# Kernel optimization log

Measured on AMD Instinct MI355X. Metric: run time of the kernel, lower is better.

## Reference

```python
import jax, jax.numpy as jnp
import numpy as np

L, T, B, N = 4, 8, 32, 65536          # layers, terms/layer, batch, flat weight size
D_K = D_V = 64; H = 8; RANK = 8       # from encoder_weight_spec
FEAT_IN = 7 * T * L                   # 224
OUT = D_K * RANK * H                  # 4096


def setup_inputs() -> dict:
    key = jax.random.key(0)
    ks = jax.random.split(key, 16)
    s = 0.05
    return {
        "wsfeat": jax.random.normal(ks[0], (L, T, B, 1, N), jnp.float32),
        "fn_W1": jax.random.normal(ks[1], (FEAT_IN, 64), jnp.float32) * s,
        "fn_b1": jnp.zeros((64,), jnp.float32),
        "ln_g": jnp.ones((64,), jnp.float32),
        "ln_b": jnp.zeros((64,), jnp.float32),
        "fn_W2": jax.random.normal(ks[2], (64, 32), jnp.float32) * s,
        "fn_b2": jnp.zeros((32,), jnp.float32),
        "MU_W": jax.random.normal(ks[3], (L, 32, OUT), jnp.float32) * s,
        "MU_b": jnp.zeros((L, OUT), jnp.float32),
        "MV_W": jax.random.normal(ks[4], (L, 32, OUT), jnp.float32) * s,
        "MV_b": jnp.zeros((L, OUT), jnp.float32),
        "NU_W": jax.random.normal(ks[5], (L, 32, OUT), jnp.float32) * s,
        "NU_b": jnp.zeros((L, OUT), jnp.float32),
        "NV_W": jax.random.normal(ks[6], (L, 32, OUT), jnp.float32) * s,
        "NV_b": jnp.zeros((L, OUT), jnp.float32),
    }


def _forward(wsfeat, fn_W1, fn_b1, ln_g, ln_b, fn_W2, fn_b2,
             MU_W, MU_b, MV_W, MV_b, NU_W, NU_b, NV_W, NV_b):
    quantiles = jnp.array([0.0, 0.25, 0.5, 0.75, 1.0], wsfeat.dtype)
    # per-term stats over last axis: mean, unbiased var, 5 linear-interp quantiles
    mean = wsfeat.mean(-1)                       # [L,T,B,1]
    var = wsfeat.var(-1, ddof=1)                 # torch.var default: unbiased
    q = jnp.quantile(wsfeat, quantiles, axis=-1)  # [5,L,T,B,1]
    feats = jnp.concatenate([mean[None], var[None], q], axis=0)  # [7,L,T,B,1]
    # original cat order: layer-major, then term, then the 7 stats
    x = jnp.transpose(feats, (3, 4, 1, 2, 0)).reshape(B, 1, L * T * 7)
    # feature_net: Linear -> LayerNorm -> GELU(exact) -> Linear
    h1 = x @ fn_W1 + fn_b1
    mu = h1.mean(-1, keepdims=True)
    v = h1.var(-1, keepdims=True)                # LayerNorm uses biased var
    h1 = (h1 - mu) / jnp.sqrt(v + 1e-5) * ln_g + ln_b
    h1 = jax.nn.gelu(h1, approximate=False)      # torch default GELU is exact erf
    feat = (h1 @ fn_W2 + fn_b2).reshape(B, 32)

    eye_scale = jnp.asarray(0.1, feat.dtype)

    def lowrank(UW, Ub, VW, Vb, D):
        # per-layer Linear(32 -> D*rank*h), vectorized over L
        U = (jnp.einsum('bf,lfo->lbo', feat, UW) + Ub[:, None, :]).reshape(L, B, H, D, RANK)
        V = (jnp.einsum('bf,lfo->lbo', feat, VW) + Vb[:, None, :]).reshape(L, B, H, RANK, D)
        M = jnp.einsum('lbhdr,lbhre->lbhde', U, V)
        return M + eye_scale * jnp.eye(D, dtype=feat.dtype)
    all_M = lowrank(MU_W, MU_b, MV_W, MV_b, D_K)  # [L,B,H,D_k,D_k]
    all_N = lowrank(NU_W, NU_b, NV_W, NV_b, D_V)  # [L,B,H,D_v,D_v]
    return all_M, all_N


def reference(wsfeat, fn_W1, fn_b1, ln_g, ln_b, fn_W2, fn_b2,
              MU_W, MU_b, MV_W, MV_b, NU_W, NU_b, NV_W, NV_b):
    return _forward(wsfeat, fn_W1, fn_b1, ln_g, ln_b, fn_W2, fn_b2,
                    MU_W, MU_b, MV_W, MV_b, NU_W, NU_b, NV_W, NV_b)
```

## Files before the change

kernel.cpp:

```cpp
#include <hip/hip_runtime.h>
#include <math.h>
#include <float.h>

#define SNT 512
#define NT 256
#define N_ROW 65536
#define B_ 32
#define L_ 4
#define T_ 8
#define H_ 8
#define OUT_ 4096
#define CAPW 2560
#define CAPB 512

#define LO0 -0.7095f
#define HI0 -0.6395f
#define LO1 -0.0350f
#define HI1  0.0350f
#define LO2  0.6395f
#define HI2  0.7095f
#define SBS (128.0f / 0.07f)

__device__ __forceinline__ unsigned f2k(float f) {
    unsigned u = __float_as_uint(f);
    return (u & 0x80000000u) ? ~u : (u | 0x80000000u);
}
__device__ __forceinline__ float k2f(unsigned k) {
    unsigned u = (k & 0x80000000u) ? (k ^ 0x80000000u) : ~k;
    return __uint_as_float(u);
}

__global__ __launch_bounds__(SNT, 8) void stats_kernel(const float* __restrict__ in,
                                                       float* __restrict__ x_ws) {
    const int row = blockIdx.x;
    const int tid = threadIdx.x;
    const int wid = tid >> 6;
    const int lane = tid & 63;
    const float4* __restrict__ p4 = (const float4*)(in + (size_t)row * N_ROW);

    __shared__ float cand[3][CAPW];
    __shared__ float bbuf[CAPB];
    __shared__ unsigned shist[128];
    __shared__ unsigned warpsum[8];
    __shared__ float4 redw[8];
    __shared__ int s_wcnt[3];
    __shared__ int s_cb[3];
    __shared__ int s_flag[6];
    __shared__ float s_qv[6];
    __shared__ int s_bc;
    __shared__ unsigned s_bidx, s_brem, s_bcnt;
    __shared__ unsigned s_dig, s_rdig;

    const unsigned ranks[6] = {16383u, 16384u, 32767u, 32768u, 49151u, 49152u};

    if (tid < 3) { s_wcnt[tid] = 0; s_cb[tid] = 0; }
    __syncthreads();

    float s = 0.f, s2 = 0.f, mn = FLT_MAX, mx = -FLT_MAX;
    int cb0 = 0, cb1 = 0, cb2 = 0;

    auto proc = [&](float x) {
        s += x; s2 = fmaf(x, x, s2);
        mn = fminf(mn, x); mx = fmaxf(mx, x);
        bool b0 = x < LO0, b1 = x < LO1, b2 = x < LO2;
        bool h0 = x < HI0, h1 = x < HI1, h2 = x < HI2;
        cb0 += b0; cb1 += b1; cb2 += b2;
        bool w0 = h0 && !b0, w1 = h1 && !b1, w2 = h2 && !b2;
        if (w0 || w1 || w2) {
            int w = w1 ? 1 : (w2 ? 2 : 0);
            int t = atomicAdd(&s_wcnt[w], 1);
            if (t < CAPW) cand[w][t] = x;
        }
    };

    for (int it = 0; it < N_ROW / 4 / SNT / 4; it++) {
        int base = it * 4 * SNT + tid;
        float4 v0 = p4[base];
        float4 v1 = p4[base + SNT];
        float4 v2 = p4[base + 2 * SNT];
        float4 v3 = p4[base + 3 * SNT];
        proc(v0.x); proc(v0.y); proc(v0.z); proc(v0.w);
        proc(v1.x); proc(v1.y); proc(v1.z); proc(v1.w);
        proc(v2.x); proc(v2.y); proc(v2.z); proc(v2.w);
        proc(v3.x); proc(v3.y); proc(v3.z); proc(v3.w);
    }

#pragma unroll
    for (int off = 32; off > 0; off >>= 1) {
        s += __shfl_xor(s, off);
        s2 += __shfl_xor(s2, off);
        mn = fminf(mn, __shfl_xor(mn, off));
        mx = fmaxf(mx, __shfl_xor(mx, off));
        cb0 += __shfl_xor(cb0, off);
        cb1 += __shfl_xor(cb1, off);
        cb2 += __shfl_xor(cb2, off);
    }
    if (lane == 0) {
        redw[wid] = make_float4(s, s2, mn, mx);
        atomicAdd(&s_cb[0], cb0);
        atomicAdd(&s_cb[1], cb1);
        atomicAdd(&s_cb[2], cb2);
    }
    __syncthreads();
    if (tid == 0) {
        float4 a = redw[0];
#pragma unroll
        for (int w = 1; w < 8; w++) {
            float4 b = redw[w];
            a.x += b.x; a.y += b.y;
            a.z = fminf(a.z, b.z); a.w = fmaxf(a.w, b.w);
        }
        redw[0] = a;
        for (int i = 0; i < 6; i++) {
            int w = i >> 1;
            long rl = (long)ranks[i] - (long)s_cb[w];
            int ok = (rl >= 0) && (rl < (long)s_wcnt[w]) && (s_wcnt[w] <= CAPW);
            s_flag[i] = !ok;
        }
    }
    __syncthreads();

    const float wlo[3] = {LO0, LO1, LO2};
    for (int w = 0; w < 3; w++) {
        if (s_flag[2 * w] && s_flag[2 * w + 1]) continue;
        int c = s_wcnt[w];
        float lo = wlo[w];
        if (tid < 128) shist[tid] = 0u;
        __syncthreads();
        for (int j = tid; j < c; j += SNT) {
            int sb = (int)((cand[w][j] - lo) * SBS);
            sb = sb < 0 ? 0 : (sb > 127 ? 127 : sb);
            atomicAdd(&shist[sb], 1u);
        }
        __syncthreads();
        if (wid == 0) {
            unsigned a0 = shist[2 * lane], a1 = shist[2 * lane + 1];
            unsigned t = a0 + a1, sc = t;
#pragma unroll
            for (int d = 1; d < 64; d <<= 1) {
                unsigned n = __shfl_up(sc, d);
                if (lane >= d) sc += n;
            }
            unsigned ex = sc - t;
            shist[2 * lane] = ex + a0;
            shist[2 * lane + 1] = ex + a0 + a1;
        }
        __syncthreads();
        for (int ii = 0; ii < 2; ii++) {
            int i = 2 * w + ii;
            if (s_flag[i]) continue;
            unsigned rl = ranks[i] - (unsigned)s_cb[w];
            if (tid < 128) {
                unsigned cc = shist[tid];
                unsigned cbp = tid ? shist[tid - 1] : 0u;
                if (rl < cc && rl >= cbp) {
                    s_bidx = (unsigned)tid; s_brem = rl - cbp; s_bcnt = cc - cbp;
                }
            }
            if (tid == 0) s_bc = 0;
            __syncthreads();
            if (s_bcnt > CAPB) {
                if (tid == 0) s_flag[i] = 1;
                __syncthreads();
                continue;
            }
            unsigned bidx = s_bidx;
            for (int j = tid; j < c; j += SNT) {
                float x = cand[w][j];
                int sb = (int)((x - lo) * SBS);
                sb = sb < 0 ? 0 : (sb > 127 ? 127 : sb);
                if ((unsigned)sb == bidx) { int q = atomicAdd(&s_bc, 1); bbuf[q] = x; }
            }
            __syncthreads();
            int bc = s_bc;
            unsigned rem = s_brem;
            for (int j = tid; j < bc; j += SNT) {
                float x = bbuf[j];
                int less = 0, eq = 0;
                for (int k = 0; k < bc; k++) {
                    float y = bbuf[k];
                    less += (y < x); eq += (y == x);
                }
                if ((unsigned)less <= rem && rem < (unsigned)(less + eq)) s_qv[i] = x;
            }
            __syncthreads();
        }
    }

    {
        unsigned* h2 = (unsigned*)&cand[0][0];
        for (int i = 0; i < 6; i++) {
            if (!s_flag[i]) continue;
            unsigned rank = ranks[i];
            unsigned prefix = 0;
            for (int level = 0; level < 3; level++) {
                int nb = (level == 2) ? 1024 : 2048;
                for (int j = tid; j < nb; j += SNT) h2[j] = 0u;
                __syncthreads();
                for (int j = tid; j < N_ROW / 4; j += SNT) {
                    float4 v = p4[j];
                    float xs[4] = {v.x, v.y, v.z, v.w};
#pragma unroll
                    for (int k = 0; k < 4; k++) {
                        unsigned key = f2k(xs[k]);
                        if (level == 0) atomicAdd(&h2[key >> 21], 1u);
                        else if (level == 1) { if ((key >> 21) == prefix) atomicAdd(&h2[(key >> 10) & 2047u], 1u); }
                        else { if ((key >> 10) == prefix) atomicAdd(&h2[key & 1023u], 1u); }
                    }
                }
                __syncthreads();
                int per = nb / SNT;
                unsigned ls[4]; unsigned acc = 0;
                int base = tid * per;
                for (int k = 0; k < per; k++) { acc += h2[base + k]; ls[k] = acc; }
                unsigned sc = acc;
#pragma unroll
                for (int d = 1; d < 64; d <<= 1) {
                    unsigned n = __shfl_up(sc, d);
                    if (lane >= d) sc += n;
                }
                if (lane == 63) warpsum[wid] = sc;
                __syncthreads();
                unsigned woff = 0;
                for (int ww = 0; ww < wid; ww++) woff += warpsum[ww];
                unsigned ex = woff + sc - acc;
                for (int k = 0; k < per; k++) h2[base + k] = ls[k] + ex;
                __syncthreads();
                for (int k = 0; k < per; k++) {
                    int j = base + k;
                    unsigned cc = h2[j];
                    unsigned cbp = j ? h2[j - 1] : 0u;
                    if (rank < cc && rank >= cbp) { s_dig = (unsigned)j; s_rdig = rank - cbp; }
                }
                __syncthreads();
                unsigned dig = s_dig;
                rank = s_rdig;
                prefix = (level == 0) ? dig : ((prefix << 11) | dig);
                __syncthreads();
            }
            if (tid == 0) s_qv[i] = k2f(prefix);
            __syncthreads();
        }
    }

    if (tid == 0) {
        double ssum = (double)redw[0].x;
        double ssq = (double)redw[0].y;
        float mean = (float)(ssum / 65536.0);
        float var = (float)((ssq - ssum * ssum / 65536.0) / 65535.0);
        float q25 = s_qv[0] + 0.75f * (s_qv[1] - s_qv[0]);
        float q50 = s_qv[2] + 0.5f * (s_qv[3] - s_qv[2]);
        float q75 = s_qv[4] + 0.25f * (s_qv[5] - s_qv[4]);
        int lt = row / B_;
        int b = row % B_;
        float* o = x_ws + b * 224 + lt * 7;
        o[0] = mean; o[1] = var; o[2] = redw[0].z;
        o[3] = q25;  o[4] = q50; o[5] = q75; o[6] = redw[0].w;
    }
}

__global__ __launch_bounds__(64) void featnet_kernel(
    const float* __restrict__ x_ws,
    const float* __restrict__ W1, const float* __restrict__ b1,
    const float* __restrict__ lng, const float* __restrict__ lnb,
    const float* __restrict__ W2, const float* __restrict__ b2,
    float* __restrict__ feat_ws) {
    int b = blockIdx.x;
    int j = threadIdx.x;
    __shared__ float xs[224];
    __shared__ float h1s[64];
    const float* x = x_ws + b * 224;
    for (int k = j; k < 224; k += 64) xs[k] = x[k];
    __syncthreads();
    float acc = b1[j];
    for (int k = 0; k < 224; k++) acc += xs[k] * W1[k * 64 + j];
    float s = acc, s2 = acc * acc;
    for (int off = 32; off > 0; off >>= 1) {
        s += __shfl_xor(s, off);
        s2 += __shfl_xor(s2, off);
    }
    float mu = s * (1.f / 64.f);
    float var = s2 * (1.f / 64.f) - mu * mu;
    float hn = (acc - mu) * rsqrtf(var + 1e-5f) * lng[j] + lnb[j];
    float ge = 0.5f * hn * (1.f + erff(hn * 0.70710678118654752f));
    h1s[j] = ge;
    __syncthreads();
    if (j < 32) {
        float a2 = b2[j];
        for (int k = 0; k < 64; k++) a2 += h1s[k] * W2[k * 32 + j];
        feat_ws[b * 32 + j] = a2;
    }
}

__global__ __launch_bounds__(NT) void lowrank_kernel(
    const float* __restrict__ feat,
    const float* __restrict__ MU_W, const float* __restrict__ MU_b,
    const float* __restrict__ MV_W, const float* __restrict__ MV_b,
    const float* __restrict__ NU_W, const float* __restrict__ NU_b,
    const float* __restrict__ NV_W, const float* __restrict__ NV_b,
    float* __restrict__ out) {
    int id = blockIdx.x;
    int l = id >> 8;
    int b = (id >> 3) & 31;
    int h = id & 7;
    int tid = threadIdx.x;

    __shared__ float fs[32];
    __shared__ float UM[512], VM[512], UN[512], VN[512];
    if (tid < 32) fs[tid] = feat[b * 32 + tid];
    __syncthreads();

    size_t woff = (size_t)l * 32 * OUT_ + (size_t)h * 512;
    size_t boff = (size_t)l * OUT_ + (size_t)h * 512;

    const float* Ws[4] = {MU_W, MV_W, NU_W, NV_W};
    const float* Bs[4] = {MU_b, MV_b, NU_b, NV_b};
    float* Ds[4] = {UM, VM, UN, VN};
#pragma unroll
    for (int m = 0; m < 4; m++) {
        const float* W = Ws[m] + woff;
        const float* Bv = Bs[m] + boff;
        float* D = Ds[m];
        for (int idx = tid; idx < 512; idx += NT) {
            float acc = Bv[idx];
#pragma unroll
            for (int f = 0; f < 32; f++) acc += fs[f] * W[(size_t)f * OUT_ + idx];
            D[idx] = acc;
        }
    }
    __syncthreads();

    int d = tid >> 2;
    int eb = (tid & 3) * 16;
    size_t obase = (size_t)id * 4096 + (size_t)d * 64 + eb;
    float* outN = out + (size_t)L_ * B_ * H_ * 4096;

    for (int e = 0; e < 16; e++) {
        float acc = 0.f;
#pragma unroll
        for (int r = 0; r < 8; r++) acc += UM[d * 8 + r] * VM[r * 64 + eb + e];
        if (d == eb + e) acc += 0.1f;
        out[obase + e] = acc;
    }
    for (int e = 0; e < 16; e++) {
        float acc = 0.f;
#pragma unroll
        for (int r = 0; r < 8; r++) acc += UN[d * 8 + r] * VN[r * 64 + eb + e];
        if (d == eb + e) acc += 0.1f;
        outN[obase + e] = acc;
    }
}

extern "C" void kernel_launch(void* const* d_in, const int* in_sizes, int n_in,
                              void* d_out, int out_size, void* d_ws, size_t ws_size,
                              hipStream_t stream) {
    const float* wsfeat = (const float*)d_in[0];
    const float* fn_W1 = (const float*)d_in[1];
    const float* fn_b1 = (const float*)d_in[2];
    const float* ln_g = (const float*)d_in[3];
    const float* ln_b = (const float*)d_in[4];
    const float* fn_W2 = (const float*)d_in[5];
    const float* fn_b2 = (const float*)d_in[6];
    const float* MU_W = (const float*)d_in[7];
    const float* MU_b = (const float*)d_in[8];
    const float* MV_W = (const float*)d_in[9];
    const float* MV_b = (const float*)d_in[10];
    const float* NU_W = (const float*)d_in[11];
    const float* NU_b = (const float*)d_in[12];
    const float* NV_W = (const float*)d_in[13];
    const float* NV_b = (const float*)d_in[14];

    float* x_ws = (float*)d_ws;
    float* feat_ws = x_ws + 32 * 224;

    stats_kernel<<<L_ * T_ * B_, SNT, 0, stream>>>(wsfeat, x_ws);
    featnet_kernel<<<B_, 64, 0, stream>>>(x_ws, fn_W1, fn_b1, ln_g, ln_b, fn_W2, fn_b2, feat_ws);
    lowrank_kernel<<<L_ * B_ * H_, NT, 0, stream>>>(feat_ws, MU_W, MU_b, MV_W, MV_b,
                                                    NU_W, NU_b, NV_W, NV_b, (float*)d_out);
}
```

Before: 113.2 us.

## Split row stats across segment blocks and batch U/V projection across batch

The per-row stats pass is split into four segment blocks per row, each writing partial sums, counts and window candidates to global workspace, and a second select kernel then merges them and does the quantile selection. This raises parallelism for the bandwidth-bound streaming pass. The low-rank stage is split into a uv_kernel that computes U/V for all batches from a shared-memory tile of weights, so each weight is read once per layer/column tile instead of once per batch, plus an expand kernel for the outer products. The cost is extra launches, a memset, global atomics, and round-trips through workspace.

```diff
diff --git a/kernel.cpp b/kernel.cpp
--- a/kernel.cpp
+++ b/kernel.cpp
@@ -2,15 +2,17 @@
 #include <math.h>
 #include <float.h>
 
-#define SNT 512
-#define NT 256
+#define TNT 256
 #define N_ROW 65536
+#define NSEG 4
+#define SEGN (N_ROW / NSEG)
 #define B_ 32
 #define L_ 4
 #define T_ 8
 #define H_ 8
 #define OUT_ 4096
 #define CAPW 2560
+#define CAPS 768
 #define CAPB 512
 
 #define LO0 -0.7095f
@@ -21,6 +23,14 @@
 #define HI2  0.7095f
 #define SBS (128.0f / 0.07f)
 
+#define XWS_OFF  0
+#define FEAT_OFF 7168
+#define PART_OFF 8192
+#define WCNT_OFF 40960
+#define CAND_OFF 49152
+#define UV_OFF   (49152 + 1024*3*CAPW)
+#define UV_MSTRIDE ((size_t)L_ * B_ * OUT_)
+
 __device__ __forceinline__ unsigned f2k(float f) {
     unsigned u = __float_as_uint(f);
     return (u & 0x80000000u) ? ~u : (u | 0x80000000u);
@@ -30,30 +40,25 @@
     return __uint_as_float(u);
 }
 
-__global__ __launch_bounds__(SNT, 8) void stats_kernel(const float* __restrict__ in,
-                                                       float* __restrict__ x_ws) {
-    const int row = blockIdx.x;
+__global__ __launch_bounds__(TNT) void stream_kernel(const float* __restrict__ in,
+                                                     float* __restrict__ ws) {
+    const int bid = blockIdx.x;
+    const int row = bid >> 2;
+    const int seg = bid & 3;
     const int tid = threadIdx.x;
     const int wid = tid >> 6;
     const int lane = tid & 63;
-    const float4* __restrict__ p4 = (const float4*)(in + (size_t)row * N_ROW);
-
-    __shared__ float cand[3][CAPW];
-    __shared__ float bbuf[CAPB];
-    __shared__ unsigned shist[128];
-    __shared__ unsigned warpsum[8];
-    __shared__ float4 redw[8];
-    __shared__ int s_wcnt[3];
-    __shared__ int s_cb[3];
-    __shared__ int s_flag[6];
-    __shared__ float s_qv[6];
-    __shared__ int s_bc;
-    __shared__ unsigned s_bidx, s_brem, s_bcnt;
-    __shared__ unsigned s_dig, s_rdig;
-
-    const unsigned ranks[6] = {16383u, 16384u, 32767u, 32768u, 49151u, 49152u};
-
-    if (tid < 3) { s_wcnt[tid] = 0; s_cb[tid] = 0; }
+    const float4* __restrict__ p4 =
+        (const float4*)(in + (size_t)row * N_ROW + (size_t)seg * SEGN);
+
+    __shared__ float cw[3][CAPS];
+    __shared__ int s_cnt[3];
+    __shared__ float4 redw[4];
+    __shared__ int redc[4][3];
+    __shared__ int s_base[3];
+    __shared__ int s_out[3];
+
+    if (tid < 3) s_cnt[tid] = 0;
     __syncthreads();
 
     float s = 0.f, s2 = 0.f, mn = FLT_MAX, mx = -FLT_MAX;
@@ -68,17 +73,17 @@
         bool w0 = h0 && !b0, w1 = h1 && !b1, w2 = h2 && !b2;
         if (w0 || w1 || w2) {
             int w = w1 ? 1 : (w2 ? 2 : 0);
-            int t = atomicAdd(&s_wcnt[w], 1);
-            if (t < CAPW) cand[w][t] = x;
+            int t = atomicAdd(&s_cnt[w], 1);
+            if (t < CAPS) cw[w][t] = x;
         }
     };
 
-    for (int it = 0; it < N_ROW / 4 / SNT / 4; it++) {
-        int base = it * 4 * SNT + tid;
+    for (int it = 0; it < SEGN / 4 / TNT / 4; it++) {
+        int base = it * 4 * TNT + tid;
         float4 v0 = p4[base];
-        float4 v1 = p4[base + SNT];
-        float4 v2 = p4[base + 2 * SNT];
-        float4 v3 = p4[base + 3 * SNT];
+        float4 v1 = p4[base + TNT];
+        float4 v2 = p4[base + 2 * TNT];
+        float4 v3 = p4[base + 3 * TNT];
         proc(v0.x); proc(v0.y); proc(v0.z); proc(v0.w);
         proc(v1.x); proc(v1.y); proc(v1.z); proc(v1.w);
         proc(v2.x); proc(v2.y); proc(v2.z); proc(v2.w);
@@ -97,38 +102,109 @@
     }
     if (lane == 0) {
         redw[wid] = make_float4(s, s2, mn, mx);
-        atomicAdd(&s_cb[0], cb0);
-        atomicAdd(&s_cb[1], cb1);
-        atomicAdd(&s_cb[2], cb2);
-    }
-    __syncthreads();
+        redc[wid][0] = cb0; redc[wid][1] = cb1; redc[wid][2] = cb2;
+    }
+    __syncthreads();
+
+    int* wcnt = (int*)ws + WCNT_OFF;
     if (tid == 0) {
         float4 a = redw[0];
-#pragma unroll
-        for (int w = 1; w < 8; w++) {
+        int c0 = redc[0][0], c1 = redc[0][1], c2 = redc[0][2];
+#pragma unroll
+        for (int w = 1; w < 4; w++) {
             float4 b = redw[w];
             a.x += b.x; a.y += b.y;
             a.z = fminf(a.z, b.z); a.w = fmaxf(a.w, b.w);
-        }
-        redw[0] = a;
+            c0 += redc[w][0]; c1 += redc[w][1]; c2 += redc[w][2];
+        }
+        float* part = ws + PART_OFF + ((size_t)row * NSEG + seg) * 8;
+        part[0] = a.x; part[1] = a.y; part[2] = a.z; part[3] = a.w;
+        part[4] = (float)c0; part[5] = (float)c1; part[6] = (float)c2;
+#pragma unroll
+        for (int w = 0; w < 3; w++) {
+            int c = s_cnt[w];
+            int over = c > CAPS;
+            s_out[w] = over ? CAPS : c;
+            s_base[w] = atomicAdd(&wcnt[row * 3 + w], over ? c + 0x00100000 : c);
+        }
+    }
+    __syncthreads();
+
+#pragma unroll
+    for (int w = 0; w < 3; w++) {
+        int c = s_out[w];
+        int base = s_base[w];
+        float* cg = ws + CAND_OFF + (size_t)(row * 3 + w) * CAPW;
+        for (int j = tid; j < c; j += TNT) {
+            int o = base + j;
+            if (o < CAPW) cg[o] = cw[w][j];
+        }
+    }
+}
+
+__global__ __launch_bounds__(TNT) void select_kernel(const float* __restrict__ in,
+                                                     float* __restrict__ ws) {
+    const int row = blockIdx.x;
+    const int tid = threadIdx.x;
+    const int wid = tid >> 6;
+    const int lane = tid & 63;
+    const float4* __restrict__ p4 = (const float4*)(in + (size_t)row * N_ROW);
+
+    __shared__ float cl[3][CAPW];
+    __shared__ float bbuf[CAPB];
+    __shared__ unsigned shist[128];
+    __shared__ unsigned warpsum[4];
+    __shared__ float4 s_red;
+    __shared__ int s_cb[3], s_wc[3];
+    __shared__ int s_flag[6];
+    __shared__ float s_qv[6];
+    __shared__ int s_bc;
+    __shared__ unsigned s_bidx, s_brem, s_bcnt;
+    __shared__ unsigned s_dig, s_rdig;
+
+    const unsigned ranks[6] = {16383u, 16384u, 32767u, 32768u, 49151u, 49152u};
+
+    if (tid == 0) {
+        const float* part = ws + PART_OFF + (size_t)row * NSEG * 8;
+        float sum = 0.f, ss2 = 0.f, mn = FLT_MAX, mx = -FLT_MAX;
+        int cb[3] = {0, 0, 0};
+        for (int g = 0; g < NSEG; g++) {
+            sum += part[g * 8 + 0]; ss2 += part[g * 8 + 1];
+            mn = fminf(mn, part[g * 8 + 2]); mx = fmaxf(mx, part[g * 8 + 3]);
+            cb[0] += (int)part[g * 8 + 4];
+            cb[1] += (int)part[g * 8 + 5];
+            cb[2] += (int)part[g * 8 + 6];
+        }
+        s_red = make_float4(sum, ss2, mn, mx);
+        const int* wcnt = (const int*)ws + WCNT_OFF;
+        for (int w = 0; w < 3; w++) { s_cb[w] = cb[w]; s_wc[w] = wcnt[row * 3 + w]; }
         for (int i = 0; i < 6; i++) {
             int w = i >> 1;
-            long rl = (long)ranks[i] - (long)s_cb[w];
-            int ok = (rl >= 0) && (rl < (long)s_wcnt[w]) && (s_wcnt[w] <= CAPW);
+            long rl = (long)ranks[i] - (long)cb[w];
+            int ok = (rl >= 0) && (rl < (long)s_wc[w]) && (s_wc[w] <= CAPW);
             s_flag[i] = !ok;
         }
+    }
+    __syncthreads();
+
+#pragma unroll
+    for (int w = 0; w < 3; w++) {
+        if (s_flag[2 * w] && s_flag[2 * w + 1]) continue;
+        int c = s_wc[w];
+        const float* cg = ws + CAND_OFF + (size_t)(row * 3 + w) * CAPW;
+        for (int j = tid; j < c; j += TNT) cl[w][j] = cg[j];
     }
     __syncthreads();
 
     const float wlo[3] = {LO0, LO1, LO2};
     for (int w = 0; w < 3; w++) {
         if (s_flag[2 * w] && s_flag[2 * w + 1]) continue;
-        int c = s_wcnt[w];
+        int c = s_wc[w];
         float lo = wlo[w];
         if (tid < 128) shist[tid] = 0u;
         __syncthreads();
-        for (int j = tid; j < c; j += SNT) {
-            int sb = (int)((cand[w][j] - lo) * SBS);
+        for (int j = tid; j < c; j += TNT) {
+            int sb = (int)((cl[w][j] - lo) * SBS);
             sb = sb < 0 ? 0 : (sb > 127 ? 127 : sb);
             atomicAdd(&shist[sb], 1u);
         }
@@ -165,8 +241,8 @@
                 continue;
             }
             unsigned bidx = s_bidx;
-            for (int j = tid; j < c; j += SNT) {
-                float x = cand[w][j];
+            for (int j = tid; j < c; j += TNT) {
+                float x = cl[w][j];
                 int sb = (int)((x - lo) * SBS);
                 sb = sb < 0 ? 0 : (sb > 127 ? 127 : sb);
                 if ((unsigned)sb == bidx) { int q = atomicAdd(&s_bc, 1); bbuf[q] = x; }
@@ -174,7 +250,7 @@
             __syncthreads();
             int bc = s_bc;
             unsigned rem = s_brem;
-            for (int j = tid; j < bc; j += SNT) {
+            for (int j = tid; j < bc; j += TNT) {
                 float x = bbuf[j];
                 int less = 0, eq = 0;
                 for (int k = 0; k < bc; k++) {
@@ -188,16 +264,16 @@
     }
 
     {
-        unsigned* h2 = (unsigned*)&cand[0][0];
+        unsigned* h2 = (unsigned*)&cl[0][0];
         for (int i = 0; i < 6; i++) {
             if (!s_flag[i]) continue;
             unsigned rank = ranks[i];
             unsigned prefix = 0;
             for (int level = 0; level < 3; level++) {
                 int nb = (level == 2) ? 1024 : 2048;
-                for (int j = tid; j < nb; j += SNT) h2[j] = 0u;
-                __syncthreads();
-                for (int j = tid; j < N_ROW / 4; j += SNT) {
+                for (int j = tid; j < nb; j += TNT) h2[j] = 0u;
+                __syncthreads();
+                for (int j = tid; j < N_ROW / 4; j += TNT) {
                     float4 v = p4[j];
                     float xs[4] = {v.x, v.y, v.z, v.w};
 #pragma unroll
@@ -209,8 +285,8 @@
                     }
                 }
                 __syncthreads();
-                int per = nb / SNT;
-                unsigned ls[4]; unsigned acc = 0;
+                int per = nb / TNT;
+                unsigned ls[8]; unsigned acc = 0;
                 int base = tid * per;
                 for (int k = 0; k < per; k++) { acc += h2[base + k]; ls[k] = acc; }
                 unsigned sc = acc;
@@ -244,8 +320,8 @@
     }
 
     if (tid == 0) {
-        double ssum = (double)redw[0].x;
-        double ssq = (double)redw[0].y;
+        double ssum = (double)s_red.x;
+        double ssq = (double)s_red.y;
         float mean = (float)(ssum / 65536.0);
         float var = (float)((ssq - ssum * ssum / 65536.0) / 65535.0);
         float q25 = s_qv[0] + 0.75f * (s_qv[1] - s_qv[0]);
@@ -253,14 +329,14 @@
         float q75 = s_qv[4] + 0.25f * (s_qv[5] - s_qv[4]);
         int lt = row / B_;
         int b = row % B_;
-        float* o = x_ws + b * 224 + lt * 7;
-        o[0] = mean; o[1] = var; o[2] = redw[0].z;
-        o[3] = q25;  o[4] = q50; o[5] = q75; o[6] = redw[0].w;
+        float* o = ws + XWS_OFF + b * 224 + lt * 7;
+        o[0] = mean; o[1] = var; o[2] = s_red.z;
+        o[3] = q25;  o[4] = q50; o[5] = q75; o[6] = s_red.w;
     }
 }
 
 __global__ __launch_bounds__(64) void featnet_kernel(
-    const float* __restrict__ x_ws,
+    const float* __restrict__ ws_in,
     const float* __restrict__ W1, const float* __restrict__ b1,
     const float* __restrict__ lng, const float* __restrict__ lnb,
     const float* __restrict__ W2, const float* __restrict__ b2,
@@ -269,7 +345,7 @@
     int j = threadIdx.x;
     __shared__ float xs[224];
     __shared__ float h1s[64];
-    const float* x = x_ws + b * 224;
+    const float* x = ws_in + XWS_OFF + b * 224;
     for (int k = j; k < 224; k += 64) xs[k] = x[k];
     __syncthreads();
     float acc = b1[j];
@@ -292,41 +368,65 @@
     }
 }
 
-__global__ __launch_bounds__(NT) void lowrank_kernel(
+__global__ __launch_bounds__(TNT) void uv_kernel(
     const float* __restrict__ feat,
     const float* __restrict__ MU_W, const float* __restrict__ MU_b,
     const float* __restrict__ MV_W, const float* __restrict__ MV_b,
     const float* __restrict__ NU_W, const float* __restrict__ NU_b,
     const float* __restrict__ NV_W, const float* __restrict__ NV_b,
-    float* __restrict__ out) {
-    int id = blockIdx.x;
-    int l = id >> 8;
-    int b = (id >> 3) & 31;
-    int h = id & 7;
-    int tid = threadIdx.x;
-
-    __shared__ float fs[32];
-    __shared__ float UM[512], VM[512], UN[512], VN[512];
-    if (tid < 32) fs[tid] = feat[b * 32 + tid];
-    __syncthreads();
-
-    size_t woff = (size_t)l * 32 * OUT_ + (size_t)h * 512;
-    size_t boff = (size_t)l * OUT_ + (size_t)h * 512;
+    float* __restrict__ uv) {
+    const int bid = blockIdx.x;
+    const int l = bid >> 5;
+    const int c0 = (bid & 31) * 128;
+    const int tid = threadIdx.x;
+
+    __shared__ float fs[32][32];
+    __shared__ float Wt[32][128];
+
+    for (int i = tid; i < 1024; i += TNT) fs[i >> 5][i & 31] = feat[i];
 
     const float* Ws[4] = {MU_W, MV_W, NU_W, NV_W};
     const float* Bs[4] = {MU_b, MV_b, NU_b, NV_b};
-    float* Ds[4] = {UM, VM, UN, VN};
+
+    const int col = tid & 127;
+    const int bh = tid >> 7;
+
 #pragma unroll
     for (int m = 0; m < 4; m++) {
-        const float* W = Ws[m] + woff;
-        const float* Bv = Bs[m] + boff;
-        float* D = Ds[m];
-        for (int idx = tid; idx < 512; idx += NT) {
-            float acc = Bv[idx];
-#pragma unroll
-            for (int f = 0; f < 32; f++) acc += fs[f] * W[(size_t)f * OUT_ + idx];
-            D[idx] = acc;
-        }
+        const float* W = Ws[m] + (size_t)l * 32 * OUT_ + c0;
+        __syncthreads();
+        for (int i = tid; i < 32 * 128; i += TNT) {
+            int f = i >> 7, c = i & 127;
+            Wt[f][c] = W[(size_t)f * OUT_ + c];
+        }
+        __syncthreads();
+        float bias = Bs[m][(size_t)l * OUT_ + c0 + col];
+        float* dst = uv + (size_t)m * UV_MSTRIDE + (size_t)l * B_ * OUT_ + c0 + col;
+        for (int k = 0; k < 16; k++) {
+            int b = bh * 16 + k;
+            float acc = bias;
+#pragma unroll
+            for (int f = 0; f < 32; f++) acc += fs[b][f] * Wt[f][col];
+            dst[(size_t)b * OUT_] = acc;
+        }
+    }
+}
+
+__global__ __launch_bounds__(TNT) void expand_kernel(const float* __restrict__ uv,
+                                                     float* __restrict__ out) {
+    const int id = blockIdx.x;
+    const int l = id >> 8;
+    const int b = (id >> 3) & 31;
+    const int h = id & 7;
+    const int tid = threadIdx.x;
+
+    __shared__ float UM[512], VM[512], UN[512], VN[512];
+    size_t base_lb = (size_t)l * B_ * OUT_ + (size_t)b * OUT_ + (size_t)h * 512;
+    for (int i = tid; i < 512; i += TNT) {
+        UM[i] = uv[0 * UV_MSTRIDE + base_lb + i];
+        VM[i] = uv[1 * UV_MSTRIDE + base_lb + i];
+        UN[i] = uv[2 * UV_MSTRIDE + base_lb + i];
+        VN[i] = uv[3 * UV_MSTRIDE + base_lb + i];
     }
     __syncthreads();
 
@@ -370,11 +470,16 @@
     const float* NV_W = (const float*)d_in[13];
     const float* NV_b = (const float*)d_in[14];
 
-    float* x_ws = (float*)d_ws;
-    float* feat_ws = x_ws + 32 * 224;
-
-    stats_kernel<<<L_ * T_ * B_, SNT, 0, stream>>>(wsfeat, x_ws);
-    featnet_kernel<<<B_, 64, 0, stream>>>(x_ws, fn_W1, fn_b1, ln_g, ln_b, fn_W2, fn_b2, feat_ws);
-    lowrank_kernel<<<L_ * B_ * H_, NT, 0, stream>>>(feat_ws, MU_W, MU_b, MV_W, MV_b,
-                                                    NU_W, NU_b, NV_W, NV_b, (float*)d_out);
-}
+    float* ws = (float*)d_ws;
+    float* feat_ws = ws + FEAT_OFF;
+    float* uv = ws + UV_OFF;
+
+    hipMemsetAsync(ws + WCNT_OFF, 0, 1024 * 3 * sizeof(int), stream);
+
+    stream_kernel<<<L_ * T_ * B_ * NSEG, TNT, 0, stream>>>(wsfeat, ws);
+    select_kernel<<<L_ * T_ * B_, TNT, 0, stream>>>(wsfeat, ws);
+    featnet_kernel<<<B_, 64, 0, stream>>>(ws, fn_W1, fn_b1, ln_g, ln_b, fn_W2, fn_b2, feat_ws);
+    uv_kernel<<<L_ * 32, TNT, 0, stream>>>(feat_ws, MU_W, MU_b, MV_W, MV_b,
+                                           NU_W, NU_b, NV_W, NV_b, uv);
+    expand_kernel<<<L_ * B_ * H_, TNT, 0, stream>>>(uv, (float*)d_out);
+}
```

Measured after the change: 155.5 us. 1.37x slower.

## Split lowrank into batched UV projection and expand kernels to reuse weights

Applied to the files above, without the earlier changes.

Replaces the per-(l,b,h) lowrank kernel, which re-read the 32xOUT weight slices once per batch element, with a uv_kernel. That kernel stages a 32x128 weight tile in shared memory and reuses it across all 32 batch rows, writing U/V to a workspace. A separate expand_kernel then loads U/V from the workspace and computes the rank-8 outer products. The aim is to cut redundant global weight traffic by 32x. In exchange it adds an extra kernel launch and a workspace write and read of 2MB.

```diff
diff --git a/kernel.cpp b/kernel.cpp
--- a/kernel.cpp
+++ b/kernel.cpp
@@ -3,7 +3,7 @@
 #include <float.h>
 
 #define SNT 512
-#define NT 256
+#define TNT 256
 #define N_ROW 65536
 #define B_ 32
 #define L_ 4
@@ -20,6 +20,11 @@
 #define LO2  0.6395f
 #define HI2  0.7095f
 #define SBS (128.0f / 0.07f)
+
+#define XWS_OFF  0
+#define FEAT_OFF 7168
+#define UV_OFF   8192
+#define UV_MSTRIDE ((size_t)L_ * B_ * OUT_)
 
 __device__ __forceinline__ unsigned f2k(float f) {
     unsigned u = __float_as_uint(f);
@@ -253,14 +258,14 @@
         float q75 = s_qv[4] + 0.25f * (s_qv[5] - s_qv[4]);
         int lt = row / B_;
         int b = row % B_;
-        float* o = x_ws + b * 224 + lt * 7;
+        float* o = x_ws + XWS_OFF + b * 224 + lt * 7;
         o[0] = mean; o[1] = var; o[2] = redw[0].z;
         o[3] = q25;  o[4] = q50; o[5] = q75; o[6] = redw[0].w;
     }
 }
 
 __global__ __launch_bounds__(64) void featnet_kernel(
-    const float* __restrict__ x_ws,
+    const float* __restrict__ ws_in,
     const float* __restrict__ W1, const float* __restrict__ b1,
     const float* __restrict__ lng, const float* __restrict__ lnb,
     const float* __restrict__ W2, const float* __restrict__ b2,
@@ -269,7 +274,7 @@
     int j = threadIdx.x;
     __shared__ float xs[224];
     __shared__ float h1s[64];
-    const float* x = x_ws + b * 224;
+    const float* x = ws_in + XWS_OFF + b * 224;
     for (int k = j; k < 224; k += 64) xs[k] = x[k];
     __syncthreads();
     float acc = b1[j];
@@ -292,41 +297,64 @@
     }
 }
 
-__global__ __launch_bounds__(NT) void lowrank_kernel(
+__global__ __launch_bounds__(TNT) void uv_kernel(
     const float* __restrict__ feat,
     const float* __restrict__ MU_W, const float* __restrict__ MU_b,
     const float* __restrict__ MV_W, const float* __restrict__ MV_b,
     const float* __restrict__ NU_W, const float* __restrict__ NU_b,
     const float* __restrict__ NV_W, const float* __restrict__ NV_b,
-    float* __restrict__ out) {
-    int id = blockIdx.x;
-    int l = id >> 8;
-    int b = (id >> 3) & 31;
-    int h = id & 7;
-    int tid = threadIdx.x;
-
-    __shared__ float fs[32];
+    float* __restrict__ uv) {
+    const int bid = blockIdx.x;
+    const int m = bid >> 7;
+    const int l = (bid >> 5) & 3;
+    const int c0 = (bid & 31) * 128;
+    const int tid = threadIdx.x;
+
+    __shared__ float fs[32][32];
+    __shared__ float Wt[32][128];
+
+    const float* W; const float* Bv;
+    if (m == 0)      { W = MU_W; Bv = MU_b; }
+    else if (m == 1) { W = MV_W; Bv = MV_b; }
+    else if (m == 2) { W = NU_W; Bv = NU_b; }
+    else             { W = NV_W; Bv = NV_b; }
+    W += (size_t)l * 32 * OUT_ + c0;
+
+    for (int i = tid; i < 1024; i += TNT) fs[i >> 5][i & 31] = feat[i];
+    for (int i = tid; i < 32 * 128; i += TNT) {
+        int f = i >> 7, c = i & 127;
+        Wt[f][c] = W[(size_t)f * OUT_ + c];
+    }
+    __syncthreads();
+
+    const int col = tid & 127;
+    const int bh = tid >> 7;
+    float bias = Bv[(size_t)l * OUT_ + c0 + col];
+    float* dst = uv + (size_t)m * UV_MSTRIDE + (size_t)l * B_ * OUT_ + c0 + col;
+    for (int k = 0; k < 16; k++) {
+        int b = bh * 16 + k;
+        float acc = bias;
+#pragma unroll
+        for (int f = 0; f < 32; f++) acc += fs[b][f] * Wt[f][col];
+        dst[(size_t)b * OUT_] = acc;
+    }
+}
+
+__global__ __launch_bounds__(TNT) void expand_kernel(const float* __restrict__ uv,
+                                                     float* __restrict__ out) {
+    const int id = blockIdx.x;
+    const int l = id >> 8;
+    const int b = (id >> 3) & 31;
+    const int h = id & 7;
+    const int tid = threadIdx.x;
+
     __shared__ float UM[512], VM[512], UN[512], VN[512];
-    if (tid < 32) fs[tid] = feat[b * 32 + tid];
-    __syncthreads();
-
-    size_t woff = (size_t)l * 32 * OUT_ + (size_t)h * 512;
-    size_t boff = (size_t)l * OUT_ + (size_t)h * 512;
-
-    const float* Ws[4] = {MU_W, MV_W, NU_W, NV_W};
-    const float* Bs[4] = {MU_b, MV_b, NU_b, NV_b};
-    float* Ds[4] = {UM, VM, UN, VN};
-#pragma unroll
-    for (int m = 0; m < 4; m++) {
-        const float* W = Ws[m] + woff;
-        const float* Bv = Bs[m] + boff;
-        float* D = Ds[m];
-        for (int idx = tid; idx < 512; idx += NT) {
-            float acc = Bv[idx];
-#pragma unroll
-            for (int f = 0; f < 32; f++) acc += fs[f] * W[(size_t)f * OUT_ + idx];
-            D[idx] = acc;
-        }
+    size_t base_lb = (size_t)l * B_ * OUT_ + (size_t)b * OUT_ + (size_t)h * 512;
+    for (int i = tid; i < 512; i += TNT) {
+        UM[i] = uv[0 * UV_MSTRIDE + base_lb + i];
+        VM[i] = uv[1 * UV_MSTRIDE + base_lb + i];
+        UN[i] = uv[2 * UV_MSTRIDE + base_lb + i];
+        VN[i] = uv[3 * UV_MSTRIDE + base_lb + i];
     }
     __syncthreads();
 
@@ -370,11 +398,13 @@
     const float* NV_W = (const float*)d_in[13];
     const float* NV_b = (const float*)d_in[14];
 
-    float* x_ws = (float*)d_ws;
-    float* feat_ws = x_ws + 32 * 224;
-
-    stats_kernel<<<L_ * T_ * B_, SNT, 0, stream>>>(wsfeat, x_ws);
-    featnet_kernel<<<B_, 64, 0, stream>>>(x_ws, fn_W1, fn_b1, ln_g, ln_b, fn_W2, fn_b2, feat_ws);
-    lowrank_kernel<<<L_ * B_ * H_, NT, 0, stream>>>(feat_ws, MU_W, MU_b, MV_W, MV_b,
-                                                    NU_W, NU_b, NV_W, NV_b, (float*)d_out);
-}
+    float* ws = (float*)d_ws;
+    float* feat_ws = ws + FEAT_OFF;
+    float* uv = ws + UV_OFF;
+
+    stats_kernel<<<L_ * T_ * B_, SNT, 0, stream>>>(wsfeat, ws);
+    featnet_kernel<<<B_, 64, 0, stream>>>(ws, fn_W1, fn_b1, ln_g, ln_b, fn_W2, fn_b2, feat_ws);
+    uv_kernel<<<4 * L_ * 32, TNT, 0, stream>>>(feat_ws, MU_W, MU_b, MV_W, MV_b,
+                                               NU_W, NU_b, NV_W, NV_b, uv);
+    expand_kernel<<<L_ * B_ * H_, TNT, 0, stream>>>(uv, (float*)d_out);
+}
```

Measured after the change: 108.6 us. 1.04x faster.
